# Optimization experiments

Measured on AMD Instinct MI355X. Metric: run time of the kernel, lower is better.

## Reference

```python
import jax, jax.numpy as jnp
import numpy as np
from jax import lax

C = 256

def conv1x1(x, w, b):
    # x: [B,C,H,W], w: [O,C], b: [O]
    return jnp.einsum('bchw,oc->bohw', x, w) + b[None, :, None, None]

def conv3x3_s2(x, w, b):
    # x: [B,C,H,W], w: [O,C,3,3] -> stride 2, pad 1
    y = lax.conv_general_dilated(x, w, window_strides=(2, 2),
                                 padding=((1, 1), (1, 1)),
                                 dimension_numbers=('NCHW', 'OIHW', 'NCHW'))
    return y + b[None, :, None, None]

def to_qv(x):
    # [B,C,H,W] -> permute(0,2,3,1) -> view [B,H,W,1,C]
    return jnp.transpose(x, (0, 2, 3, 1))[:, :, :, None, :]

def to_k(x):
    # [B,C,H,W] -> permute(0,2,3,1) -> view [B,H,W,C,1]
    return jnp.transpose(x, (0, 2, 3, 1))[:, :, :, :, None]

def upsample2x_nearest(x):
    return jnp.repeat(jnp.repeat(x, 2, axis=2), 2, axis=3)


def setup_inputs() -> dict:
    key = jax.random.key(0)
    ks = jax.random.split(key, 20)
    x1 = jax.random.normal(ks[0], (2, C, 128, 128), dtype=jnp.float32)
    x2 = jax.random.normal(ks[1], (2, C, 64, 64), dtype=jnp.float32)
    s = 0.05
    d = {'x1': x1, 'x2': x2}
    names = ['q1', 'q2', 'ks1', 'ks2', 'kup', 'v1', 'v2']
    for i, n in enumerate(names):
        d[n + '_w'] = jax.random.normal(ks[2 + 2 * i], (C, C), dtype=jnp.float32) * s
        d[n + '_b'] = jax.random.normal(ks[3 + 2 * i], (C,), dtype=jnp.float32) * s
    d['kdown_w'] = jax.random.normal(ks[16], (C, C, 3, 3), dtype=jnp.float32) * s
    d['kdown_b'] = jax.random.normal(ks[17], (C,), dtype=jnp.float32) * s
    return d


def reference(x1, x2, q1_w, q1_b, q2_w, q2_b, ks1_w, ks1_b, ks2_w, ks2_b,
              kup_w, kup_b, v1_w, v1_b, v2_w, v2_b, kdown_w, kdown_b):
    q1 = to_qv(conv1x1(x1, q1_w, q1_b))            # [B,128,128,1,C]
    q2 = to_qv(conv1x1(x2, q2_w, q2_b))            # [B,64,64,1,C]
    k_up = to_k(upsample2x_nearest(conv1x1(x2, kup_w, kup_b)))  # [B,128,128,C,1]
    k_self_1 = to_k(conv1x1(x1, ks1_w, ks1_b))     # [B,128,128,C,1]
    k_self_2 = to_k(conv1x1(x2, ks2_w, ks2_b))     # [B,64,64,C,1]
    k_down = to_k(conv3x3_s2(x1, kdown_w, kdown_b))  # [B,64,64,C,1]
    v1 = to_qv(conv1x1(x1, v1_w, v1_b))            # [B,128,128,1,C]
    v2 = to_qv(conv1x1(x2, v2_w, v2_b))            # [B,64,64,1,C]
    return (q1, q2, k_up, k_self_1, k_self_2, k_down, v1, v2)
```

## Files before the change

### kernel.cpp

```cpp
#include <hip/hip_runtime.h>
#include <hip/hip_bf16.h>
#include <stdint.h>


typedef __attribute__((ext_vector_type(8))) __bf16 bf16x8;
typedef __attribute__((ext_vector_type(4))) float f32x4;
typedef __attribute__((ext_vector_type(8))) unsigned short u16x8;

typedef const __attribute__((address_space(1))) uint32_t* gptr_t;
typedef __attribute__((address_space(3))) uint32_t* lptr_t;

__device__ __forceinline__ void cp16(void* lds, const void* g) {
  gptr_t gp = reinterpret_cast<gptr_t>(reinterpret_cast<uintptr_t>(g));
  lptr_t lp = reinterpret_cast<lptr_t>(
      static_cast<uint32_t>(reinterpret_cast<uintptr_t>(lds)));
  __builtin_amdgcn_global_load_lds(gp, lp, 16, 0, 0);
}

struct WArgs {
  const float* w1[7];
  const float* kdw;
};

__global__ void prep_transpose(WArgs a, const float* __restrict__ x1,
                               const float* __restrict__ x2,
                               uint16_t* __restrict__ wf,
                               uint16_t* __restrict__ x1p,
                               uint16_t* __restrict__ x2b) {
  __shared__ float tile[64][65];
  const int bx = blockIdx.x;
  const int tid = threadIdx.x;
  if (bx < 512) {
    const int idx = bx * 256 + tid;
    const int mat = idx >> 13;
    const int g = idx & 8191;
    const int jg = g >> 9;
    const int kc = (g >> 6) & 7;
    const int lane = g & 63;
    const int o = jg * 16 + (lane & 15);
    const int k0 = kc * 32 + (lane >> 4) * 8;
    float f[8];
    if (mat < 7) {
      const float* w = a.w1[mat];
      const float4 v0 = *(const float4*)(w + o * 256 + k0);
      const float4 v1 = *(const float4*)(w + o * 256 + k0 + 4);
      f[0] = v0.x; f[1] = v0.y; f[2] = v0.z; f[3] = v0.w;
      f[4] = v1.x; f[5] = v1.y; f[6] = v1.z; f[7] = v1.w;
    } else {
      const int tap = mat - 7;
#pragma unroll
      for (int e = 0; e < 8; e++)
        f[e] = a.kdw[(long)o * 2304 + (long)(k0 + e) * 9 + tap];
    }
    u16x8 u;
#pragma unroll
    for (int e = 0; e < 8; e++) {
      __hip_bfloat16 hb = __float2bfloat16(f[e]);
      u[e] = *reinterpret_cast<uint16_t*>(&hb);
    }
    *(u16x8*)(wf + (long)idx * 8) = u;
    return;
  }
  if (bx < 641) {
    const int c = (bx - 512) * 256 + tid;
    const int b = (c >= 16512) ? 1 : 0;
    const int cc = c - b * 16512;
    int h, w, g8;
    if (cc < 4160) {
      h = 0; w = cc >> 5; g8 = cc & 31;
    } else if (cc < 8320) {
      const int s = cc - 4160; h = 129; w = s >> 5; g8 = s & 31;
    } else if (cc < 12416) {
      const int s = cc - 8320; h = 1 + (s >> 5); w = 0; g8 = s & 31;
    } else {
      const int s = cc - 12416; h = 1 + (s >> 5); w = 129; g8 = s & 31;
    }
    u16x8 z = {};
    *(u16x8*)(x1p + (((long)(b * 130 + h)) * 130 + w) * 256 + g8 * 8) = z;
    return;
  }
  const int t = bx - 641;
  const float* src;
  uint16_t* dst;
  int H, W, pad, b, h, bxx, by;
  if (t < 2048) {
    src = x1; dst = x1p; H = 128; W = 128; pad = 1;
    bxx = t & 1; by = (t >> 1) & 3;
    const int z = t >> 3; b = z >> 7; h = z & 127;
  } else {
    const int t2 = t - 2048;
    src = x2; dst = x2b; H = 64; W = 64; pad = 0;
    bxx = 0; by = t2 & 3;
    const int z = t2 >> 2;
    b = z >> 6; h = z & 63;
  }
  const int wt = bxx * 64;
  const int ct = by * 64;
  const long cs = (long)H * W;
  const float* s = src + ((long)(b * 256 + ct) * H + h) * W + wt;
  const int rw = tid >> 4;
  const int rf = tid & 15;
#pragma unroll
  for (int p = 0; p < 4; p++) {
    const int cl = p * 16 + rw;
    const float4 v = *(const float4*)(s + (long)cl * cs + rf * 4);
    tile[cl][rf * 4 + 0] = v.x;
    tile[cl][rf * 4 + 1] = v.y;
    tile[cl][rf * 4 + 2] = v.z;
    tile[cl][rf * 4 + 3] = v.w;
  }
  __syncthreads();
  const int wl0 = tid >> 3;
  const int cg = tid & 7;
  const int Wp = W + 2 * pad;
  const long rowb = ((long)(b * (H + 2 * pad) + h + pad)) * Wp + pad + wt;
#pragma unroll
  for (int p = 0; p < 2; p++) {
    const int wl = p * 32 + wl0;
    u16x8 u;
#pragma unroll
    for (int k = 0; k < 8; k++) {
      __hip_bfloat16 hb = __float2bfloat16(tile[cg * 8 + k][wl]);
      u[k] = *reinterpret_cast<uint16_t*>(&hb);
    }
    *(u16x8*)(dst + (rowb + wl) * 256 + ct + cg * 8) = u;
  }
}

struct Job {
  const uint16_t* A;
  const uint16_t* Wf;
  const float* bias;
  float* out;
  int start;
  int mode;
};
struct JobArgs {
  Job j[8];
};

__global__ __launch_bounds__(256, 2) void fused_gemm(JobArgs args) {
  int jid = 0;
#pragma unroll
  for (int t = 1; t < 8; t++)
    if ((int)blockIdx.x >= args.j[t].start) jid = t;
  const Job jb = args.j[jid];
  const int bid = blockIdx.x - jb.start;
  const int mode = jb.mode;

  __shared__ __align__(16) uint16_t lA[32768];

  const int tid = threadIdx.x;
  const int lane = tid & 63;
  const int wave = tid >> 6;
  const int wr = wave & 1;
  const int wc = wave >> 1;
  const int q = lane >> 4;
  const int l15 = lane & 15;
  const int ksel = ((lane & 3) ^ ((lane >> 3) & 3)) * 8;
  const int qsw = (q ^ ((l15 >> 1) & 3)) * 8;

  if (mode == 3) {
    const int mtile = bid >> 1;
    const int ntile = bid & 1;
    const int row = mtile * 64 + wave * 16 + (lane >> 2);
    const long p =
        ((long)((row >> 12) * 130 + 2 * ((row >> 6) & 63))) * 130 + 2 * (row & 63);
    const uint16_t* rowA = jb.A + p * 256 + ksel;

    f32x4 acc[2][4] = {};
    for (int tap = 0; tap < 9; tap++) {
      const int kh = tap / 3;
      const int kw = tap - kh * 3;
      const long aoff = (long)(kh * 130 + kw) * 256;
      const uint16_t* wf = jb.Wf + (long)tap * 65536;
      if (tap) __syncthreads();
#pragma unroll
      for (int kap = 0; kap < 8; kap++)
        cp16(lA + (kap * 256 + wave * 64) * 8, rowA + aoff + kap * 32);
      __syncthreads();
#pragma unroll
      for (int kc = 0; kc < 8; kc++) {
        bf16x8 av[2];
#pragma unroll
        for (int i = 0; i < 2; i++)
          av[i] = *(const bf16x8*)(lA + (kc * 64 + wr * 32 + i * 16 + l15) * 32 + qsw);
#pragma unroll
        for (int j = 0; j < 4; j++) {
          const bf16x8 bv = *(const bf16x8*)(
              wf + ((long)((ntile * 8 + wc * 4 + j) * 8 + kc) * 64 + lane) * 8);
#pragma unroll
          for (int i = 0; i < 2; i++)
            acc[i][j] = __builtin_amdgcn_mfma_f32_16x16x32_bf16(av[i], bv,
                                                                acc[i][j], 0, 0, 0);
        }
      }
    }
    const int nb = ntile * 128 + wc * 64 + l15;
    const int mb = mtile * 64 + wr * 32 + q * 4;
#pragma unroll
    for (int j = 0; j < 4; j++) {
      const int n = nb + j * 16;
      const float bvs = jb.bias[n];
#pragma unroll
      for (int i = 0; i < 2; i++) {
        const int m0 = mb + i * 16;
#pragma unroll
        for (int r = 0; r < 4; r++)
          jb.out[(long)(m0 + r) * 256 + n] = acc[i][j][r] + bvs;
      }
    }
    return;
  }

  const int mtile = bid;
  const uint16_t* rowA[2];
  {
    const int rbase = wave * 16 + (lane >> 2);
#pragma unroll
    for (int rh = 0; rh < 2; rh++) {
      const int m = mtile * 128 + rh * 64 + rbase;
      long p;
      if (mode == 0) {
        p = ((long)((m >> 14) * 130 + ((m >> 7) & 127) + 1)) * 130 + (m & 127) + 1;
      } else {
        p = m;
      }
      rowA[rh] = jb.A + p * 256 + ksel;
    }
  }

#pragma unroll
  for (int kap = 0; kap < 16; kap++)
    cp16(lA + (kap * 256 + wave * 64) * 8, rowA[kap & 1] + (kap >> 1) * 32);
  __syncthreads();

  f32x4 acc[4][8] = {};
#pragma unroll
  for (int kc = 0; kc < 8; kc++) {
    bf16x8 av[4];
#pragma unroll
    for (int i = 0; i < 4; i++)
      av[i] = *(const bf16x8*)(lA + (kc * 128 + wr * 64 + i * 16 + l15) * 32 + qsw);
#pragma unroll
    for (int j = 0; j < 8; j++) {
      const bf16x8 bv =
          *(const bf16x8*)(jb.Wf + ((long)((wc * 8 + j) * 8 + kc) * 64 + lane) * 8);
#pragma unroll
      for (int i = 0; i < 4; i++)
        acc[i][j] = __builtin_amdgcn_mfma_f32_16x16x32_bf16(av[i], bv,
                                                            acc[i][j], 0, 0, 0);
    }
  }

  const int nb = wc * 128 + l15;
  const int mb = mtile * 128 + wr * 64 + q * 4;
  if (mode == 2) {
#pragma unroll
    for (int j = 0; j < 8; j++) {
      const int n = nb + j * 16;
      const float bvs = jb.bias[n];
#pragma unroll
      for (int i = 0; i < 4; i++) {
        const int m0 = mb + i * 16;
#pragma unroll
        for (int r = 0; r < 4; r++) {
          const int m = m0 + r;
          const int b = m >> 12;
          const int h2 = (m >> 6) & 63;
          const int w2 = m & 63;
          const float val = acc[i][j][r] + bvs;
          float* o =
              jb.out + ((long)(b * 128 + 2 * h2) * 128 + 2 * w2) * 256 + n;
          o[0] = val;
          o[256] = val;
          o[32768] = val;
          o[32768 + 256] = val;
        }
      }
    }
  } else {
#pragma unroll
    for (int j = 0; j < 8; j++) {
      const int n = nb + j * 16;
      const float bvs = jb.bias[n];
#pragma unroll
      for (int i = 0; i < 4; i++) {
        const int m0 = mb + i * 16;
#pragma unroll
        for (int r = 0; r < 4; r++)
          jb.out[(long)(m0 + r) * 256 + n] = acc[i][j][r] + bvs;
      }
    }
  }
}

extern "C" void kernel_launch(void* const* d_in, const int* in_sizes, int n_in,
                              void* d_out, int out_size, void* d_ws,
                              size_t ws_size, hipStream_t stream) {
  (void)in_sizes; (void)n_in; (void)out_size; (void)ws_size;
  const float* x1 = (const float*)d_in[0];
  const float* x2 = (const float*)d_in[1];
  float* out = (float*)d_out;

  uint16_t* x1p = (uint16_t*)d_ws;
  uint16_t* x2b = x1p + 8652800;
  uint16_t* wf = x2b + 2097152;

  WArgs wa;
  wa.w1[0] = (const float*)d_in[2];
  wa.w1[1] = (const float*)d_in[4];
  wa.w1[2] = (const float*)d_in[6];
  wa.w1[3] = (const float*)d_in[8];
  wa.w1[4] = (const float*)d_in[10];
  wa.w1[5] = (const float*)d_in[12];
  wa.w1[6] = (const float*)d_in[14];
  wa.kdw = (const float*)d_in[16];
  prep_transpose<<<3201, 256, 0, stream>>>(wa, x1, x2, wf, x1p, x2b);

  JobArgs ja;
  ja.j[0] = {x1p, wf + 7 * 65536, (const float*)d_in[17], out + 29360128L, 0,    3};
  ja.j[1] = {x1p, wf + 0 * 65536, (const float*)d_in[3],  out + 0L,        256,  0};
  ja.j[2] = {x1p, wf + 2 * 65536, (const float*)d_in[7],  out + 18874368L, 512,  0};
  ja.j[3] = {x1p, wf + 5 * 65536, (const float*)d_in[13], out + 31457280L, 768,  0};
  ja.j[4] = {x2b, wf + 4 * 65536, (const float*)d_in[11], out + 10485760L, 1024, 2};
  ja.j[5] = {x2b, wf + 1 * 65536, (const float*)d_in[5],  out + 8388608L,  1088, 1};
  ja.j[6] = {x2b, wf + 3 * 65536, (const float*)d_in[9],  out + 27262976L, 1152, 1};
  ja.j[7] = {x2b, wf + 6 * 65536, (const float*)d_in[15], out + 39845888L, 1216, 1};
  fused_gemm<<<1280, 256, 0, stream>>>(ja);
}
```

Measured before the change: 291.5 us.

## Double-buffer conv3x3 tap loads and split 1x1 GEMM wait into halves

In the 3x3 stride-2 path, the A tile for the next tap is now prefetched into a second LDS buffer while MFMAs run on the current tap, replacing two barriers per tap with one wait-and-barrier. In the 1x1 GEMM path, the full vmcnt(0) sync is replaced by a partial wait (vmcnt(8)) so the first half of K can be computed while the second half of the LDS loads is still landing. This needs twice the LDS for the conv tile and relies on the hand-written vmcnt counts matching the order in which the global loads are issued.

```diff
diff --git a/kernel.cpp b/kernel.cpp
--- a/kernel.cpp
+++ b/kernel.cpp
@@ -169,31 +169,47 @@
     const uint16_t* rowA = jb.A + p * 256 + ksel;
 
     f32x4 acc[2][4] = {};
+#pragma unroll
+    for (int kap = 0; kap < 8; kap++)
+      cp16(lA + (kap * 256 + wave * 64) * 8, rowA + kap * 32);
+    asm volatile("s_waitcnt vmcnt(0)" ::: "memory");
+    __builtin_amdgcn_s_barrier();
+    asm volatile("" ::: "memory");
+
     for (int tap = 0; tap < 9; tap++) {
-      const int kh = tap / 3;
-      const int kw = tap - kh * 3;
-      const long aoff = (long)(kh * 130 + kw) * 256;
-      const uint16_t* wf = jb.Wf + (long)tap * 65536;
-      if (tap) __syncthreads();
-#pragma unroll
-      for (int kap = 0; kap < 8; kap++)
-        cp16(lA + (kap * 256 + wave * 64) * 8, rowA + aoff + kap * 32);
-      __syncthreads();
+      const int cur = (tap & 1) * 16384;
+      if (tap < 8) {
+        const int nt = tap + 1;
+        const int kh = nt / 3;
+        const int kw = nt - kh * 3;
+        const long aoff = (long)(kh * 130 + kw) * 256;
+        const int nbuf = ((tap & 1) ^ 1) * 16384;
+#pragma unroll
+        for (int kap = 0; kap < 8; kap++)
+          cp16(lA + nbuf + (kap * 256 + wave * 64) * 8, rowA + aoff + kap * 32);
+      }
+      const uint16_t* wfp = jb.Wf + (long)tap * 65536;
 #pragma unroll
       for (int kc = 0; kc < 8; kc++) {
         bf16x8 av[2];
 #pragma unroll
         for (int i = 0; i < 2; i++)
-          av[i] = *(const bf16x8*)(lA + (kc * 64 + wr * 32 + i * 16 + l15) * 32 + qsw);
+          av[i] = *(const bf16x8*)(lA + cur +
+                                   (kc * 64 + wr * 32 + i * 16 + l15) * 32 + qsw);
 #pragma unroll
         for (int j = 0; j < 4; j++) {
           const bf16x8 bv = *(const bf16x8*)(
-              wf + ((long)((ntile * 8 + wc * 4 + j) * 8 + kc) * 64 + lane) * 8);
+              wfp + ((long)((ntile * 8 + wc * 4 + j) * 8 + kc) * 64 + lane) * 8);
 #pragma unroll
           for (int i = 0; i < 2; i++)
             acc[i][j] = __builtin_amdgcn_mfma_f32_16x16x32_bf16(av[i], bv,
                                                                 acc[i][j], 0, 0, 0);
         }
+      }
+      if (tap < 8) {
+        asm volatile("s_waitcnt vmcnt(0)" ::: "memory");
+        __builtin_amdgcn_s_barrier();
+        asm volatile("" ::: "memory");
       }
     }
     const int nb = ntile * 128 + wc * 64 + l15;
@@ -233,23 +249,33 @@
 #pragma unroll
   for (int kap = 0; kap < 16; kap++)
     cp16(lA + (kap * 256 + wave * 64) * 8, rowA[kap & 1] + (kap >> 1) * 32);
-  __syncthreads();
 
   f32x4 acc[4][8] = {};
 #pragma unroll
-  for (int kc = 0; kc < 8; kc++) {
-    bf16x8 av[4];
-#pragma unroll
-    for (int i = 0; i < 4; i++)
-      av[i] = *(const bf16x8*)(lA + (kc * 128 + wr * 64 + i * 16 + l15) * 32 + qsw);
-#pragma unroll
-    for (int j = 0; j < 8; j++) {
-      const bf16x8 bv =
-          *(const bf16x8*)(jb.Wf + ((long)((wc * 8 + j) * 8 + kc) * 64 + lane) * 8);
+  for (int half = 0; half < 2; half++) {
+    if (half == 0) {
+      asm volatile("s_waitcnt vmcnt(8)" ::: "memory");
+    } else {
+      asm volatile("s_waitcnt vmcnt(0)" ::: "memory");
+    }
+    __builtin_amdgcn_s_barrier();
+    asm volatile("" ::: "memory");
+#pragma unroll
+    for (int kk = 0; kk < 4; kk++) {
+      const int kc = half * 4 + kk;
+      bf16x8 av[4];
 #pragma unroll
       for (int i = 0; i < 4; i++)
-        acc[i][j] = __builtin_amdgcn_mfma_f32_16x16x32_bf16(av[i], bv,
-                                                            acc[i][j], 0, 0, 0);
+        av[i] = *(const bf16x8*)(lA + (kc * 128 + wr * 64 + i * 16 + l15) * 32 + qsw);
+#pragma unroll
+      for (int j = 0; j < 8; j++) {
+        const bf16x8 bv =
+            *(const bf16x8*)(jb.Wf + ((long)((wc * 8 + j) * 8 + kc) * 64 + lane) * 8);
+#pragma unroll
+        for (int i = 0; i < 4; i++)
+          acc[i][j] = __builtin_amdgcn_mfma_f32_16x16x32_bf16(av[i], bv,
+                                                              acc[i][j], 0, 0, 0);
+      }
     }
   }
 
```

Result: slower. 298.4 us (+2.4%).
